# Optimization experiments

Measured on AMD Instinct MI355X. Metric: run time of the kernel, lower is better.

## Reference

```python
import jax, jax.numpy as jnp
import numpy as np


def _conv3x3(x, w, b):
    # standard 3x3 conv, stride 1, pad 1, NCHW/OIHW
    out = jax.lax.conv_general_dilated(
        x, w, window_strides=(1, 1), padding=((1, 1), (1, 1)),
        dimension_numbers=('NCHW', 'OIHW', 'NCHW'))
    return out + b[None, :, None, None]


def _deform_conv3x3(x, offsets, w, b):
    # torchvision DeformConv2d, kernel 3x3, stride 1, pad 1, dilation 1,
    # conv groups == offset groups == OG, zero padding for out-of-bounds samples.
    B, C, H, W = x.shape
    K = 9  # 3x3 taps
    OG = offsets.shape[1] // (2 * K)
    Cg = C // OG
    # offsets layout: [B, OG*K*2, H, W] with 2 = (dy, dx)
    off = offsets.reshape(B, OG, K, 2, H, W)
    ky = (jnp.arange(K) // 3 - 1).astype(x.dtype).reshape(1, 1, K, 1, 1)
    kx = (jnp.arange(K) % 3 - 1).astype(x.dtype).reshape(1, 1, K, 1, 1)
    # sampling positions per output pixel and tap: [B, OG, K, H, W]
    py = off[:, :, :, 0] + ky + jnp.arange(H, dtype=x.dtype).reshape(1, 1, 1, H, 1)
    px = off[:, :, :, 1] + kx + jnp.arange(W, dtype=x.dtype).reshape(1, 1, 1, 1, W)
    y0 = jnp.floor(py)
    x0 = jnp.floor(px)
    x_g = x.reshape(B, OG, Cg, H * W)
    acc = jnp.zeros((B, OG, Cg, K, H, W), dtype=x.dtype)
    # bilinear interpolation: accumulate 4 corners, masking out-of-bounds to zero
    for yy, xx in ((y0, x0), (y0, x0 + 1), (y0 + 1, x0), (y0 + 1, x0 + 1)):
        wgt = (1.0 - jnp.abs(py - yy)) * (1.0 - jnp.abs(px - xx))
        valid = ((yy >= 0) & (yy < H) & (xx >= 0) & (xx < W)).astype(x.dtype)
        yi = jnp.clip(yy, 0, H - 1).astype(jnp.int32)
        xi = jnp.clip(xx, 0, W - 1).astype(jnp.int32)
        idx = (yi * W + xi).reshape(B, OG, 1, K * H * W)
        idx = jnp.broadcast_to(idx, (B, OG, Cg, K * H * W))
        vals = jnp.take_along_axis(x_g, idx, axis=-1).reshape(B, OG, Cg, K, H, W)
        acc = acc + vals * (wgt * valid)[:, :, None]
    # grouped conv over sampled patches: w is [C_out, C_in/OG, 3, 3]
    wk = w.reshape(OG, Cg, Cg, K)  # (group, out-per-group, in-per-group, tap)
    out = jnp.einsum('bgckhw,gock->bgohw', acc, wk).reshape(B, C, H, W)
    return out + b[None, :, None, None]


def setup_inputs() -> dict:
    key = jax.random.key(0)
    k0, k1, k2, k3 = jax.random.split(key, 4)
    B, C, H, W, OG = 8, 256, 64, 64, 4
    x = jax.random.normal(k0, (B, C, H, W), jnp.float32)
    # small offset-conv weights so predicted offsets stay in a realistic range
    w_off = jax.random.normal(k1, (2 * 9 * OG, C, 3, 3), jnp.float32) * 0.01
    b_off = jnp.zeros((2 * 9 * OG,), jnp.float32)
    fan_in = (C // OG) * 9
    w_def = jax.random.normal(k2, (C, C // OG, 3, 3), jnp.float32) * (1.0 / np.sqrt(fan_in))
    b_def = jax.random.normal(k3, (C,), jnp.float32) * 0.01
    return {"x": x, "w_off": w_off, "b_off": b_off, "w_def": w_def, "b_def": b_def}


def reference(x, w_off, b_off, w_def, b_def):
    offsets = _conv3x3(x, w_off, b_off)
    return _deform_conv3x3(x, offsets, w_def, b_def)
```

## Files before the change

### kernel.cpp

```cpp
#include <hip/hip_runtime.h>
#include <hip/hip_bf16.h>

#define BATCH 8
#define CIN   256
#define HH    64
#define WW    64
#define HW    4096
#define OG    4
#define CG    64
#define COFF  72

typedef __attribute__((ext_vector_type(8))) _Float16 half8;
typedef __attribute__((ext_vector_type(4))) float floatx4;

static __device__ __forceinline__ half8 splat8(float f) {
    _Float16 h = (_Float16)f;
    return (half8){h, h, h, h, h, h, h, h};
}

#define OFFS_ELEMS (BATCH * COFF * HH * WW)
#define WT_ELEMS   (OG * 9 * 4 * 2 * 64 * 8)
#define WO3_ELEMS  (8 * 9 * 5 * 64 * 8)
#define XH_BYTE_OFF ((size_t)OFFS_ELEMS * 4 + (size_t)WT_ELEMS * 2 + (size_t)WO3_ELEMS * 2)
#define NEED_NHWC (XH_BYTE_OFF + (size_t)BATCH * HW * CIN * 2)

#define PREPW_BLOCKS (((WT_ELEMS + WO3_ELEMS) + 255) / 256)

__global__ __launch_bounds__(256) void prep_kernel(
    const float* __restrict__ x, const float* __restrict__ w_def,
    const float* __restrict__ w_off, _Float16* __restrict__ xh,
    _Float16* __restrict__ wT3, _Float16* __restrict__ woT3)
{
    const int t = threadIdx.x;
    if (blockIdx.x >= 512) {
        int i = (blockIdx.x - 512) * 256 + t;
        if (i < WT_ELEMS) {
            int j = i & 7;
            int l = (i >> 3) & 63;
            int rest = i >> 9;
            int kh = rest & 1;
            int mt = (rest >> 1) & 3;
            int gk = rest >> 3;
            int k = gk % 9, g = gk / 9;
            int o = mt * 16 + (l & 15);
            int c = kh * 32 + (l >> 4) * 8 + j;
            wT3[i] = (_Float16)w_def[((size_t)((g * CG + o) * CG + c)) * 9 + k];
        } else if (i < WT_ELEMS + WO3_ELEMS) {
            int idx = i - WT_ELEMS;
            int j = idx & 7;
            int l = (idx >> 3) & 63;
            int rest = idx >> 9;
            int mt = rest % 5;
            int ct = rest / 5;
            int tap = ct % 9, chunk = ct / 9;
            int o = mt * 16 + (l & 15);
            int c = chunk * 32 + (l >> 4) * 8 + j;
            float v = (o < COFF) ? w_off[((size_t)(o * CIN + c)) * 9 + tap] : 0.f;
            woT3[idx] = (_Float16)v;
        }
        return;
    }

    const int b = blockIdx.x >> 6;
    const int y = blockIdx.x & 63;

    __shared__ short tile[64][258];

#pragma unroll
    for (int it = 0; it < 16; ++it) {
        int i  = t + it * 256;
        int c  = i >> 4;
        int p4 = (i & 15) << 2;
        float4 v = *(const float4*)(x + (((size_t)(b * CIN + c)) << 12) + (y << 6) + p4);
        tile[p4 + 0][c] = __builtin_bit_cast(short, (_Float16)v.x);
        tile[p4 + 1][c] = __builtin_bit_cast(short, (_Float16)v.y);
        tile[p4 + 2][c] = __builtin_bit_cast(short, (_Float16)v.z);
        tile[p4 + 3][c] = __builtin_bit_cast(short, (_Float16)v.w);
    }
    __syncthreads();

    _Float16* dst = xh + (((size_t)(b * HW)) << 8) + ((size_t)(y * WW) << 8);
#pragma unroll
    for (int k = 0; k < 8; ++k) {
        int i  = t + k * 256;
        int p  = i >> 5;
        int c8 = (i & 31) << 3;
        const unsigned* tp = (const unsigned*)&tile[p][c8];
        uint4 r = make_uint4(tp[0], tp[1], tp[2], tp[3]);
        *(uint4*)(dst + ((size_t)p << 8) + c8) = r;
    }
}

__global__ __launch_bounds__(512) void conv_off_nhwc(
    const _Float16* __restrict__ xh, const _Float16* __restrict__ woT3,
    const float* __restrict__ b_off, float* __restrict__ offs)
{
    const int b  = blockIdx.x >> 5;
    const int h0 = (blockIdx.x & 31) << 1;
    const int t  = threadIdx.x;
    const int wv = t >> 6;
    const int l  = t & 63;
    const int lane16 = l & 15;
    const int quad   = l >> 4;
    const int nh = wv & 1;
    const int ks = wv >> 1;

    __shared__ _Float16 xs[4][66][256];

    floatx4 acc[5][4];
#pragma unroll
    for (int mt = 0; mt < 5; ++mt)
#pragma unroll
        for (int nf = 0; nf < 4; ++nf) acc[mt][nf] = (floatx4){0.f, 0.f, 0.f, 0.f};

#pragma unroll
    for (int i = 0; i < 16; ++i) {
        int f    = (i << 9) + t;
        int r    = f >> 11;
        int px   = (f >> 5) & 63;
        int slot = f & 31;
        int yy   = h0 - 1 + r;
        uint4 v = make_uint4(0, 0, 0, 0);
        if ((unsigned)yy < 64u)
            v = *(const uint4*)(xh + (((size_t)(b * HW + (yy << 6) + px)) << 8)
                                   + (slot << 3));
        int rec = px + 1;
        *(uint4*)&xs[r][rec][(slot ^ (rec & 7)) << 3] = v;
    }
    if (t < 256) {
        int r = t >> 6, side = (t >> 5) & 1, slot = t & 31;
        int rec = side * 65;
        *(uint4*)&xs[r][rec][(slot ^ (rec & 7)) << 3] = make_uint4(0, 0, 0, 0);
    }
    __syncthreads();

#pragma unroll
    for (int ch2 = 0; ch2 < 2; ++ch2) {
        const int ch = ks * 2 + ch2;
#pragma unroll
        for (int tap = 0; tap < 9; ++tap) {
            const int ky = tap / 3, kx = tap % 3;

            const _Float16* ab = woT3 + (((size_t)((ch * 9 + tap) * 5)) << 9) + (l << 3);
            half8 a0 = *(const half8*)(ab);
            half8 a1 = *(const half8*)(ab + 512);
            half8 a2 = *(const half8*)(ab + 1024);
            half8 a3 = *(const half8*)(ab + 1536);
            half8 a4 = *(const half8*)(ab + 2048);

            half8 bf[4];
#pragma unroll
            for (int nf = 0; nf < 4; ++nf) {
                int rec  = nf * 16 + lane16 + kx;
                int slot = (ch * 4 + quad) ^ (rec & 7);
                bf[nf] = *(const half8*)&xs[nh + ky][rec][slot << 3];
            }

#pragma unroll
            for (int nf = 0; nf < 4; ++nf) {
                acc[0][nf] = __builtin_amdgcn_mfma_f32_16x16x32_f16(a0, bf[nf], acc[0][nf], 0, 0, 0);
                acc[1][nf] = __builtin_amdgcn_mfma_f32_16x16x32_f16(a1, bf[nf], acc[1][nf], 0, 0, 0);
                acc[2][nf] = __builtin_amdgcn_mfma_f32_16x16x32_f16(a2, bf[nf], acc[2][nf], 0, 0, 0);
                acc[3][nf] = __builtin_amdgcn_mfma_f32_16x16x32_f16(a3, bf[nf], acc[3][nf], 0, 0, 0);
                acc[4][nf] = __builtin_amdgcn_mfma_f32_16x16x32_f16(a4, bf[nf], acc[4][nf], 0, 0, 0);
            }
        }
    }

    __syncthreads();
    float* red = (float*)&xs[0][0][0];

    if (ks != 0) {
        float* dst = red + (size_t)(((ks - 1) * 2 + nh) * 5120) + (l << 2);
#pragma unroll
        for (int mt = 0; mt < 5; ++mt)
#pragma unroll
            for (int nf = 0; nf < 4; ++nf)
                *(floatx4*)&dst[(mt * 4 + nf) * 256] = acc[mt][nf];
    }
    __syncthreads();

    if (ks == 0) {
#pragma unroll
        for (int s = 0; s < 3; ++s) {
            const float* src = red + (size_t)((s * 2 + nh) * 5120) + (l << 2);
#pragma unroll
            for (int mt = 0; mt < 5; ++mt)
#pragma unroll
                for (int nf = 0; nf < 4; ++nf)
                    acc[mt][nf] += *(const floatx4*)&src[(mt * 4 + nf) * 256];
        }
        const int y = h0 + nh;
#pragma unroll
        for (int mt = 0; mt < 5; ++mt) {
#pragma unroll
            for (int rg = 0; rg < 4; ++rg) {
                int oc = mt * 16 + quad * 4 + rg;
                if (oc < COFF) {
                    float bias = b_off[oc];
#pragma unroll
                    for (int nf = 0; nf < 4; ++nf)
                        offs[(((size_t)(b * COFF + oc)) << 12) + (y << 6) + nf * 16 + lane16] =
                            acc[mt][nf][rg] + bias;
                }
            }
        }
    }
}

__global__ __launch_bounds__(512) void deform_nhwc(
    const _Float16* __restrict__ xh, const float* __restrict__ offs,
    const _Float16* __restrict__ wT3, const float* __restrict__ b_def,
    float* __restrict__ out)
{
    const int hh = blockIdx.x & 31;
    const int bg = blockIdx.x >> 5;
    const int g  = bg & 3;
    const int b  = bg >> 2;
    const int h0 = hh << 1;
    const int t  = threadIdx.x;
    const int wv = t >> 6;
    const int l  = t & 63;
    const int lane16 = l & 15;
    const int quad   = l >> 4;
    const int p  = (wv & 3) * 16 + lane16;
    const int hw = h0 + (wv >> 2);

    __shared__ _Float16 ls[6 * 64 * 64];
    __shared__ _Float16 wa2[2][4096];

    floatx4 acc[4];
#pragma unroll
    for (int mt = 0; mt < 4; ++mt) acc[mt] = (floatx4){0.f, 0.f, 0.f, 0.f};

#pragma unroll
    for (int it = 0; it < 6; ++it) {
        int id  = it * 512 + t;
        int c16 = id & 7;
        int px  = (id >> 3) & 63;
        int r   = id >> 9;
        int r_img = h0 - 2 + r;
        uint4 v = make_uint4(0, 0, 0, 0);
        if ((unsigned)r_img < 64u)
            v = *(const uint4*)(xh + (((size_t)(b * HW + (r_img << 6) + px)) << 8)
                                   + g * 64 + c16 * 8);
        *(uint4*)&ls[((r * 64 + px) << 6) + ((c16 ^ (px & 7)) << 3)] = v;
    }

    {
        const uint4* asrc = (const uint4*)(wT3 + ((size_t)(g * 9) << 12));
        uint4 a0 = asrc[t];
        *(uint4*)&wa2[0][t * 8] = a0;
    }

    float dyv[9], dxv[9];
    {
        const float* ofb = offs + (((size_t)(b * COFF + g * 18)) * HH + hw) * WW + p;
#pragma unroll
        for (int k = 0; k < 9; ++k) {
            dyv[k] = ofb[(size_t)(2 * k) * HW];
            dxv[k] = ofb[(size_t)(2 * k + 1) * HW];
        }
    }

    __syncthreads();

    const _Float16* xg = xh + (((size_t)(b * HW)) << 8) + g * 64;

#pragma unroll
    for (int k = 0; k < 9; ++k) {
        uint4 pw0;
        if (k < 8) {
            const uint4* asrc = (const uint4*)(wT3 + ((size_t)(g * 9 + k + 1) << 12));
            pw0 = asrc[t];
        }

        float py = dyv[k] + (float)(hw + (k / 3) - 1);
        float px_ = dxv[k] + (float)(p + (k % 3) - 1);
        float y0f = floorf(py), x0f = floorf(px_);
        float fy = py - y0f, fx = px_ - x0f;
        int y0 = (int)y0f, x0 = (int)x0f;
        float wy0 = ((y0 >= 0) & (y0 < HH)) ? (1.f - fy) : 0.f;
        float wy1 = ((y0 >= -1) & (y0 < HH - 1)) ? fy : 0.f;
        float wx0 = ((x0 >= 0) & (x0 < WW)) ? (1.f - fx) : 0.f;
        float wx1 = ((x0 >= -1) & (x0 < WW - 1)) ? fx : 0.f;
        int yia = min(max(y0, 0), HH - 1), yib = min(max(y0 + 1, 0), HH - 1);
        int xia = min(max(x0, 0), WW - 1), xib = min(max(x0 + 1, 0), WW - 1);
        bool inWin = (y0 >= h0 - 2) & (y0 <= h0 + 2);

        int wa_ = min(max(yia - (h0 - 2), 0), 5);
        int wb_ = min(max(yib - (h0 - 2), 0), 5);

        int soa = (quad ^ (xia & 7)) << 3;
        int sob = (quad ^ (xib & 7)) << 3;
        const _Float16* pa = ls + ((wa_ * 64 + xia) << 6);
        const _Float16* pb = ls + ((wa_ * 64 + xib) << 6);
        const _Float16* pc = ls + ((wb_ * 64 + xia) << 6);
        const _Float16* pd = ls + ((wb_ * 64 + xib) << 6);

        half8 aL = *(const half8*)(pa + soa);
        half8 bL = *(const half8*)(pb + sob);
        half8 cL = *(const half8*)(pc + soa);
        half8 dL = *(const half8*)(pd + sob);
        half8 aH = *(const half8*)(pa + (soa ^ 32));
        half8 bH = *(const half8*)(pb + (sob ^ 32));
        half8 cH = *(const half8*)(pc + (soa ^ 32));
        half8 dH = *(const half8*)(pd + (sob ^ 32));

        if (!inWin) {
            const int co = quad * 8;
            const _Float16* qa = xg + (((size_t)((yia << 6) + xia)) << 8);
            const _Float16* qb = xg + (((size_t)((yia << 6) + xib)) << 8);
            const _Float16* qc = xg + (((size_t)((yib << 6) + xia)) << 8);
            const _Float16* qd = xg + (((size_t)((yib << 6) + xib)) << 8);
            aL = *(const half8*)(qa + co);  aH = *(const half8*)(qa + co + 32);
            bL = *(const half8*)(qb + co);  bH = *(const half8*)(qb + co + 32);
            cL = *(const half8*)(qc + co);  cH = *(const half8*)(qc + co + 32);
            dL = *(const half8*)(qd + co);  dH = *(const half8*)(qd + co + 32);
        }

        half8 W00 = splat8(wy0 * wx0), W01 = splat8(wy0 * wx1);
        half8 W10 = splat8(wy1 * wx0), W11 = splat8(wy1 * wx1);
        half8 f0 = aL * W00 + bL * W01 + cL * W10 + dL * W11;
        half8 f1 = aH * W00 + bH * W01 + cH * W10 + dH * W11;

        const _Float16* wk = &wa2[k & 1][l * 8];
#pragma unroll
        for (int mt = 0; mt < 4; ++mt) {
            half8 a0 = *(const half8*)(wk + (mt * 2 + 0) * 512);
            half8 a1 = *(const half8*)(wk + (mt * 2 + 1) * 512);
            acc[mt] = __builtin_amdgcn_mfma_f32_16x16x32_f16(a0, f0, acc[mt], 0, 0, 0);
            acc[mt] = __builtin_amdgcn_mfma_f32_16x16x32_f16(a1, f1, acc[mt], 0, 0, 0);
        }

        if (k < 8) {
            *(uint4*)&wa2[(k + 1) & 1][t * 8] = pw0;
            __syncthreads();
        }
    }

#pragma unroll
    for (int mt = 0; mt < 4; ++mt) {
#pragma unroll
        for (int rg = 0; rg < 4; ++rg) {
            int o = mt * 16 + quad * 4 + rg;
            float v = acc[mt][rg] + b_def[g * CG + o];
            out[((size_t)(b * CIN + g * CG + o) * HH + hw) * WW + p] = v;
        }
    }
}

__global__ __launch_bounds__(256) void conv_off_fb(
    const float* __restrict__ x, const float* __restrict__ w_off,
    const float* __restrict__ b_off, float* __restrict__ offs)
{
    const int b = blockIdx.x >> 6;
    const int h = blockIdx.x & 63;
    const int t = threadIdx.x;
    const int w = t & 63;
    const int q = t >> 6;

    __shared__ float xsf[3][8][WW + 2];
    __shared__ float wtf[9][8][COFF];

    float acc[18];
#pragma unroll
    for (int j = 0; j < 18; ++j) acc[j] = 0.f;

    for (int c0 = 0; c0 < CIN; c0 += 8) {
        __syncthreads();
        for (int i = t; i < 3 * 8 * (WW + 2); i += 256) {
            int wp = i % (WW + 2);
            int rem = i / (WW + 2);
            int cc = rem % 8;
            int ky = rem / 8;
            int yy = h + ky - 1;
            int xx = wp - 1;
            float v = 0.f;
            if (yy >= 0 && yy < HH && xx >= 0 && xx < WW)
                v = x[(((size_t)b * CIN + c0 + cc) * HH + yy) * WW + xx];
            xsf[ky][cc][wp] = v;
        }
        for (int i = t; i < 9 * 8 * COFF; i += 256) {
            int oc = i % COFF;
            int rem = i / COFF;
            int cc = rem % 8;
            int tap = rem / 8;
            wtf[tap][cc][oc] = w_off[((size_t)oc * CIN + c0 + cc) * 9 + tap];
        }
        __syncthreads();
        for (int tap = 0; tap < 9; ++tap) {
            const int ky = tap / 3, kx = tap % 3;
#pragma unroll
            for (int cc = 0; cc < 8; ++cc) {
                float xv = xsf[ky][cc][w + kx];
#pragma unroll
                for (int j = 0; j < 18; ++j)
                    acc[j] += xv * wtf[tap][cc][q * 18 + j];
            }
        }
    }
#pragma unroll
    for (int j = 0; j < 18; ++j) {
        int oc = q * 18 + j;
        offs[(((size_t)b * COFF + oc) * HH + h) * WW + w] = acc[j] + b_off[oc];
    }
}

__global__ __launch_bounds__(256) void deform_fb(
    const float* __restrict__ x, const float* __restrict__ offs,
    const float* __restrict__ w_def, const float* __restrict__ b_def,
    float* __restrict__ out)
{
    const int h  = blockIdx.x & 63;
    const int bg = blockIdx.x >> 6;
    const int g  = bg & 3;
    const int b  = bg >> 2;
    const int t  = threadIdx.x;
    const int w  = t & 63;
    const int q  = t >> 6;

    __shared__ float vlds[CG][WW];
    __shared__ float wt2[CG][CG];
    __shared__ int   sidx[4][WW];
    __shared__ float swgt[4][WW];

    float acc[16];
#pragma unroll
    for (int j = 0; j < 16; ++j) acc[j] = 0.f;

    const float* xg = x + ((size_t)(b * CIN + g * CG)) * HW;

    for (int k = 0; k < 9; ++k) {
        __syncthreads();
        if (t < 64) {
            const int ky = k / 3 - 1, kx = k % 3 - 1;
            size_t obase = (((size_t)b * COFF + g * 18 + k * 2) * HH + h) * WW + w;
            float dy = offs[obase];
            float dx = offs[obase + (size_t)HW];
            float py = dy + (float)(h + ky);
            float px = dx + (float)(w + kx);
            float y0 = floorf(py), x0 = floorf(px);
            float fy = py - y0, fx = px - x0;
#pragma unroll
            for (int cn = 0; cn < 4; ++cn) {
                float yy = y0 + (float)(cn >> 1);
                float xx = x0 + (float)(cn & 1);
                float wy = (cn >> 1) ? fy : (1.f - fy);
                float wx = (cn & 1) ? fx : (1.f - fx);
                bool valid = (yy >= 0.f) && (yy < (float)HH) &&
                             (xx >= 0.f) && (xx < (float)WW);
                int yi = (int)fminf(fmaxf(yy, 0.f), (float)(HH - 1));
                int xi = (int)fminf(fmaxf(xx, 0.f), (float)(WW - 1));
                sidx[cn][w] = yi * WW + xi;
                swgt[cn][w] = valid ? (wy * wx) : 0.f;
            }
        }
        for (int i = t; i < CG * CG; i += 256) {
            int o = i >> 6, c = i & 63;
            wt2[c][o] = w_def[((size_t)(g * CG + o) * CG + c) * 9 + k];
        }
        __syncthreads();

        int   i0 = sidx[0][w], i1 = sidx[1][w], i2 = sidx[2][w], i3 = sidx[3][w];
        float g0 = swgt[0][w], g1 = swgt[1][w], g2 = swgt[2][w], g3 = swgt[3][w];
#pragma unroll
        for (int j = 0; j < 16; ++j) {
            int c = q * 16 + j;
            const float* xc = xg + (size_t)c * HW;
            float v = g0 * xc[i0] + g1 * xc[i1] + g2 * xc[i2] + g3 * xc[i3];
            vlds[c][w] = v;
        }
        __syncthreads();

#pragma unroll 4
        for (int c = 0; c < CG; ++c) {
            float xv = vlds[c][w];
#pragma unroll
            for (int j = 0; j < 16; ++j)
                acc[j] += xv * wt2[c][q * 16 + j];
        }
    }

#pragma unroll
    for (int j = 0; j < 16; ++j) {
        int o = q * 16 + j;
        out[(((size_t)b * CIN + g * CG + o) * HH + h) * WW + w] =
            acc[j] + b_def[g * CG + o];
    }
}

extern "C" void kernel_launch(void* const* d_in, const int* in_sizes, int n_in,
                              void* d_out, int out_size, void* d_ws, size_t ws_size,
                              hipStream_t stream) {
    const float* x     = (const float*)d_in[0];
    const float* w_off = (const float*)d_in[1];
    const float* b_off = (const float*)d_in[2];
    const float* w_def = (const float*)d_in[3];
    const float* b_def = (const float*)d_in[4];
    float* out = (float*)d_out;

    char* ws = (char*)d_ws;
    float*     offs = (float*)ws;
    _Float16*  wT3  = (_Float16*)(ws + (size_t)OFFS_ELEMS * 4);
    _Float16*  woT3 = (_Float16*)(ws + (size_t)OFFS_ELEMS * 4 + (size_t)WT_ELEMS * 2);
    _Float16*  xh   = (_Float16*)(ws + XH_BYTE_OFF);

    if (ws_size >= NEED_NHWC) {
        prep_kernel<<<512 + PREPW_BLOCKS, 256, 0, stream>>>(x, w_def, w_off, xh, wT3, woT3);
        conv_off_nhwc<<<BATCH * 32, 512, 0, stream>>>(xh, woT3, b_off, offs);
        deform_nhwc<<<BATCH * OG * 32, 512, 0, stream>>>(xh, offs, wT3, b_def, out);
    } else {
        conv_off_fb<<<BATCH * HH, 256, 0, stream>>>(x, w_off, b_off, offs);
        deform_fb<<<BATCH * OG * HH, 256, 0, stream>>>(x, offs, w_def, b_def, out);
    }
}
```

Measured before the change: 140.8 us.

## Process four rows per deform block with per-wave register-held weight fragments

The deform kernel now covers four output rows per block instead of two, so each wave handles 32 pixels (two 16-pixel fragments). Weight A-fragments are read from global memory straight into registers each tap, replacing the double-buffered LDS weight staging and its per-tap barriers. Offsets are prefetched one tap ahead rather than all nine up front. This cuts halo row loading per output row and removes synchronisation, but it halves the grid to 512 blocks, raises LDS use to 64KB per block, and adds register pressure from the doubled accumulators and the weight fragments.

```diff
diff --git a/kernel.cpp b/kernel.cpp
--- a/kernel.cpp
+++ b/kernel.cpp
@@ -213,28 +213,29 @@
     const _Float16* __restrict__ wT3, const float* __restrict__ b_def,
     float* __restrict__ out)
 {
-    const int hh = blockIdx.x & 31;
-    const int bg = blockIdx.x >> 5;
+    const int hh = blockIdx.x & 15;
+    const int bg = blockIdx.x >> 4;
     const int g  = bg & 3;
     const int b  = bg >> 2;
-    const int h0 = hh << 1;
+    const int h0 = hh << 2;
     const int t  = threadIdx.x;
     const int wv = t >> 6;
     const int l  = t & 63;
     const int lane16 = l & 15;
     const int quad   = l >> 4;
-    const int p  = (wv & 3) * 16 + lane16;
-    const int hw = h0 + (wv >> 2);
-
-    __shared__ _Float16 ls[6 * 64 * 64];
-    __shared__ _Float16 wa2[2][4096];
-
-    floatx4 acc[4];
-#pragma unroll
-    for (int mt = 0; mt < 4; ++mt) acc[mt] = (floatx4){0.f, 0.f, 0.f, 0.f};
-
-#pragma unroll
-    for (int it = 0; it < 6; ++it) {
+    const int row = h0 + (wv >> 1);
+    const int p0  = (wv & 1) * 32 + lane16;
+
+    __shared__ _Float16 ls[8 * 64 * 64];
+
+    floatx4 acc[2][4];
+#pragma unroll
+    for (int nf = 0; nf < 2; ++nf)
+#pragma unroll
+        for (int mt = 0; mt < 4; ++mt) acc[nf][mt] = (floatx4){0.f, 0.f, 0.f, 0.f};
+
+#pragma unroll
+    for (int it = 0; it < 8; ++it) {
         int id  = it * 512 + t;
         int c16 = id & 7;
         int px  = (id >> 3) & 63;
@@ -247,105 +248,111 @@
         *(uint4*)&ls[((r * 64 + px) << 6) + ((c16 ^ (px & 7)) << 3)] = v;
     }
 
-    {
-        const uint4* asrc = (const uint4*)(wT3 + ((size_t)(g * 9) << 12));
-        uint4 a0 = asrc[t];
-        *(uint4*)&wa2[0][t * 8] = a0;
-    }
-
-    float dyv[9], dxv[9];
-    {
-        const float* ofb = offs + (((size_t)(b * COFF + g * 18)) * HH + hw) * WW + p;
-#pragma unroll
-        for (int k = 0; k < 9; ++k) {
-            dyv[k] = ofb[(size_t)(2 * k) * HW];
-            dxv[k] = ofb[(size_t)(2 * k + 1) * HW];
-        }
+    const float* ofb = offs + (((size_t)(b * COFF + g * 18)) * HH + row) * WW;
+    float dyc[2], dxc[2];
+#pragma unroll
+    for (int nf = 0; nf < 2; ++nf) {
+        dyc[nf] = ofb[p0 + nf * 16];
+        dxc[nf] = ofb[HW + p0 + nf * 16];
     }
 
     __syncthreads();
 
     const _Float16* xg = xh + (((size_t)(b * HW)) << 8) + g * 64;
+    const _Float16* wgbase = wT3 + ((size_t)(g * 9) << 12) + (l << 3);
 
 #pragma unroll
     for (int k = 0; k < 9; ++k) {
-        uint4 pw0;
+        const _Float16* wk = wgbase + ((size_t)k << 12);
+        half8 af[8];
+#pragma unroll
+        for (int f = 0; f < 8; ++f) af[f] = *(const half8*)(wk + f * 512);
+
+        float ndy[2], ndx[2];
         if (k < 8) {
-            const uint4* asrc = (const uint4*)(wT3 + ((size_t)(g * 9 + k + 1) << 12));
-            pw0 = asrc[t];
-        }
-
-        float py = dyv[k] + (float)(hw + (k / 3) - 1);
-        float px_ = dxv[k] + (float)(p + (k % 3) - 1);
-        float y0f = floorf(py), x0f = floorf(px_);
-        float fy = py - y0f, fx = px_ - x0f;
-        int y0 = (int)y0f, x0 = (int)x0f;
-        float wy0 = ((y0 >= 0) & (y0 < HH)) ? (1.f - fy) : 0.f;
-        float wy1 = ((y0 >= -1) & (y0 < HH - 1)) ? fy : 0.f;
-        float wx0 = ((x0 >= 0) & (x0 < WW)) ? (1.f - fx) : 0.f;
-        float wx1 = ((x0 >= -1) & (x0 < WW - 1)) ? fx : 0.f;
-        int yia = min(max(y0, 0), HH - 1), yib = min(max(y0 + 1, 0), HH - 1);
-        int xia = min(max(x0, 0), WW - 1), xib = min(max(x0 + 1, 0), WW - 1);
-        bool inWin = (y0 >= h0 - 2) & (y0 <= h0 + 2);
-
-        int wa_ = min(max(yia - (h0 - 2), 0), 5);
-        int wb_ = min(max(yib - (h0 - 2), 0), 5);
-
-        int soa = (quad ^ (xia & 7)) << 3;
-        int sob = (quad ^ (xib & 7)) << 3;
-        const _Float16* pa = ls + ((wa_ * 64 + xia) << 6);
-        const _Float16* pb = ls + ((wa_ * 64 + xib) << 6);
-        const _Float16* pc = ls + ((wb_ * 64 + xia) << 6);
-        const _Float16* pd = ls + ((wb_ * 64 + xib) << 6);
-
-        half8 aL = *(const half8*)(pa + soa);
-        half8 bL = *(const half8*)(pb + sob);
-        half8 cL = *(const half8*)(pc + soa);
-        half8 dL = *(const half8*)(pd + sob);
-        half8 aH = *(const half8*)(pa + (soa ^ 32));
-        half8 bH = *(const half8*)(pb + (sob ^ 32));
-        half8 cH = *(const half8*)(pc + (soa ^ 32));
-        half8 dH = *(const half8*)(pd + (sob ^ 32));
-
-        if (!inWin) {
-            const int co = quad * 8;
-            const _Float16* qa = xg + (((size_t)((yia << 6) + xia)) << 8);
-            const _Float16* qb = xg + (((size_t)((yia << 6) + xib)) << 8);
-            const _Float16* qc = xg + (((size_t)((yib << 6) + xia)) << 8);
-            const _Float16* qd = xg + (((size_t)((yib << 6) + xib)) << 8);
-            aL = *(const half8*)(qa + co);  aH = *(const half8*)(qa + co + 32);
-            bL = *(const half8*)(qb + co);  bH = *(const half8*)(qb + co + 32);
-            cL = *(const half8*)(qc + co);  cH = *(const half8*)(qc + co + 32);
-            dL = *(const half8*)(qd + co);  dH = *(const half8*)(qd + co + 32);
-        }
-
-        half8 W00 = splat8(wy0 * wx0), W01 = splat8(wy0 * wx1);
-        half8 W10 = splat8(wy1 * wx0), W11 = splat8(wy1 * wx1);
-        half8 f0 = aL * W00 + bL * W01 + cL * W10 + dL * W11;
-        half8 f1 = aH * W00 + bH * W01 + cH * W10 + dH * W11;
-
-        const _Float16* wk = &wa2[k & 1][l * 8];
+#pragma unroll
+            for (int nf = 0; nf < 2; ++nf) {
+                ndy[nf] = ofb[(size_t)(2 * k + 2) * HW + p0 + nf * 16];
+                ndx[nf] = ofb[(size_t)(2 * k + 3) * HW + p0 + nf * 16];
+            }
+        }
+
+#pragma unroll
+        for (int nf = 0; nf < 2; ++nf) {
+            const int p = p0 + nf * 16;
+
+            float py = dyc[nf] + (float)(row + (k / 3) - 1);
+            float px_ = dxc[nf] + (float)(p + (k % 3) - 1);
+            float y0f = floorf(py), x0f = floorf(px_);
+            float fy = py - y0f, fx = px_ - x0f;
+            int y0 = (int)y0f, x0 = (int)x0f;
+            float wy0 = ((y0 >= 0) & (y0 < HH)) ? (1.f - fy) : 0.f;
+            float wy1 = ((y0 >= -1) & (y0 < HH - 1)) ? fy : 0.f;
+            float wx0 = ((x0 >= 0) & (x0 < WW)) ? (1.f - fx) : 0.f;
+            float wx1 = ((x0 >= -1) & (x0 < WW - 1)) ? fx : 0.f;
+            int yia = min(max(y0, 0), HH - 1), yib = min(max(y0 + 1, 0), HH - 1);
+            int xia = min(max(x0, 0), WW - 1), xib = min(max(x0 + 1, 0), WW - 1);
+            bool inWin = (y0 >= h0 - 2) & (y0 <= h0 + 4);
+
+            int wa_ = min(max(yia - (h0 - 2), 0), 7);
+            int wb_ = min(max(yib - (h0 - 2), 0), 7);
+
+            int soa = (quad ^ (xia & 7)) << 3;
+            int sob = (quad ^ (xib & 7)) << 3;
+            const _Float16* pa = ls + ((wa_ * 64 + xia) << 6);
+            const _Float16* pb = ls + ((wa_ * 64 + xib) << 6);
+            const _Float16* pc = ls + ((wb_ * 64 + xia) << 6);
+            const _Float16* pd = ls + ((wb_ * 64 + xib) << 6);
+
+            half8 aL = *(const half8*)(pa + soa);
+            half8 bL = *(const half8*)(pb + sob);
+            half8 cL = *(const half8*)(pc + soa);
+            half8 dL = *(const half8*)(pd + sob);
+            half8 aH = *(const half8*)(pa + (soa ^ 32));
+            half8 bH = *(const half8*)(pb + (sob ^ 32));
+            half8 cH = *(const half8*)(pc + (soa ^ 32));
+            half8 dH = *(const half8*)(pd + (sob ^ 32));
+
+            if (!inWin) {
+                const int co = quad * 8;
+                const _Float16* qa = xg + (((size_t)((yia << 6) + xia)) << 8);
+                const _Float16* qb = xg + (((size_t)((yia << 6) + xib)) << 8);
+                const _Float16* qc = xg + (((size_t)((yib << 6) + xia)) << 8);
+                const _Float16* qd = xg + (((size_t)((yib << 6) + xib)) << 8);
+                aL = *(const half8*)(qa + co);  aH = *(const half8*)(qa + co + 32);
+                bL = *(const half8*)(qb + co);  bH = *(const half8*)(qb + co + 32);
+                cL = *(const half8*)(qc + co);  cH = *(const half8*)(qc + co + 32);
+                dL = *(const half8*)(qd + co);  dH = *(const half8*)(qd + co + 32);
+            }
+
+            half8 W00 = splat8(wy0 * wx0), W01 = splat8(wy0 * wx1);
+            half8 W10 = splat8(wy1 * wx0), W11 = splat8(wy1 * wx1);
+            half8 f0 = aL * W00 + bL * W01 + cL * W10 + dL * W11;
+            half8 f1 = aH * W00 + bH * W01 + cH * W10 + dH * W11;
+
+#pragma unroll
+            for (int mt = 0; mt < 4; ++mt) {
+                acc[nf][mt] = __builtin_amdgcn_mfma_f32_16x16x32_f16(af[mt * 2 + 0], f0, acc[nf][mt], 0, 0, 0);
+                acc[nf][mt] = __builtin_amdgcn_mfma_f32_16x16x32_f16(af[mt * 2 + 1], f1, acc[nf][mt], 0, 0, 0);
+            }
+        }
+
+        if (k < 8) {
+#pragma unroll
+            for (int nf = 0; nf < 2; ++nf) { dyc[nf] = ndy[nf]; dxc[nf] = ndx[nf]; }
+        }
+    }
+
+#pragma unroll
+    for (int nf = 0; nf < 2; ++nf) {
 #pragma unroll
         for (int mt = 0; mt < 4; ++mt) {
-            half8 a0 = *(const half8*)(wk + (mt * 2 + 0) * 512);
-            half8 a1 = *(const half8*)(wk + (mt * 2 + 1) * 512);
-            acc[mt] = __builtin_amdgcn_mfma_f32_16x16x32_f16(a0, f0, acc[mt], 0, 0, 0);
-            acc[mt] = __builtin_amdgcn_mfma_f32_16x16x32_f16(a1, f1, acc[mt], 0, 0, 0);
-        }
-
-        if (k < 8) {
-            *(uint4*)&wa2[(k + 1) & 1][t * 8] = pw0;
-            __syncthreads();
-        }
-    }
-
-#pragma unroll
-    for (int mt = 0; mt < 4; ++mt) {
-#pragma unroll
-        for (int rg = 0; rg < 4; ++rg) {
-            int o = mt * 16 + quad * 4 + rg;
-            float v = acc[mt][rg] + b_def[g * CG + o];
-            out[((size_t)(b * CIN + g * CG + o) * HH + hw) * WW + p] = v;
+#pragma unroll
+            for (int rg = 0; rg < 4; ++rg) {
+                int o = mt * 16 + quad * 4 + rg;
+                float v = acc[nf][mt][rg] + b_def[g * CG + o];
+                out[((size_t)(b * CIN + g * CG + o) * HH + row) * WW + p0 + nf * 16] = v;
+            }
         }
     }
 }
@@ -509,7 +516,7 @@
     if (ws_size >= NEED_NHWC) {
         prep_kernel<<<512 + PREPW_BLOCKS, 256, 0, stream>>>(x, w_def, w_off, xh, wT3, woT3);
         conv_off_nhwc<<<BATCH * 32, 512, 0, stream>>>(xh, woT3, b_off, offs);
-        deform_nhwc<<<BATCH * OG * 32, 512, 0, stream>>>(xh, offs, wT3, b_def, out);
+        deform_nhwc<<<BATCH * OG * 16, 512, 0, stream>>>(xh, offs, wT3, b_def, out);
     } else {
         conv_off_fb<<<BATCH * HH, 256, 0, stream>>>(x, w_off, b_off, offs);
         deform_fb<<<BATCH * OG * HH, 256, 0, stream>>>(x, offs, w_def, b_def, out);
```

After: 143.2 us. About the same (+1.7%).
